# Kernel tuning notes

Measured on AMD Instinct MI355X. Metric: run time of the kernel, lower is better.

Reference implementation:

```python
import jax, jax.numpy as jnp
import numpy as np

B, C, H, W = 8, 64, 64, 64
NPTS = 4096          # points per image
FX = 32              # extra per-point features
DOUT = 256
K = 3


def setup_inputs() -> dict:
    key = jax.random.key(0)
    k1, k2, k3, k4 = jax.random.split(key, 4)
    images = jax.random.normal(k1, (B, C, H, W), dtype=jnp.float32)
    x = jax.random.normal(k2, (B * NPTS, FX), dtype=jnp.float32)
    pos = jax.random.uniform(k3, (B * NPTS, 2), dtype=jnp.float32)
    batch = jnp.repeat(jnp.arange(B, dtype=jnp.int64), NPTS)
    W_nn = jax.random.normal(k4, (C + FX, DOUT), dtype=jnp.float32) / np.sqrt(C + FX)
    b_nn = jnp.zeros((DOUT,), dtype=jnp.float32)
    return {"images": images, "x": x, "pos": pos, "batch": batch,
            "W_nn": W_nn, "b_nn": b_nn, "k": K}


def reference(images, x, pos, batch, W_nn, b_nn, k):
    Bn, Cn, Hn, Wn = images.shape
    D = Hn
    P = D * D  # pixels per image
    # pixel features: [B, P, C]
    pix = jnp.transpose(images, (0, 2, 3, 1)).reshape(Bn, P, Cn)
    # pixel centers; flattened index i = r*D + c -> (centers[c], centers[r])
    centers = (jnp.arange(D, dtype=images.dtype) + 0.5) / D
    ppos = jnp.stack([jnp.tile(centers, D), jnp.repeat(centers, D)], axis=-1)  # [P, 2]
    # points are uniform per batch: [B, Npts, 2]
    pts = pos.reshape(Bn, -1, 2)
    # squared distances via |a|^2 + |b|^2 - 2 a.b -> [B, Npts, P]
    d2 = (jnp.sum(pts * pts, -1)[:, :, None]
          + jnp.sum(ppos * ppos, -1)[None, None, :]
          - 2.0 * jnp.einsum('bnd,pd->bnp', pts, ppos))
    neg_d2k, idx = jax.lax.top_k(-d2, k)            # k nearest pixels
    d2k = jnp.maximum(-neg_d2k, 1e-16)
    w = 1.0 / d2k                                    # [B, Npts, k]
    gathered = jax.vmap(lambda p, i: p[i])(pix, idx)  # [B, Npts, k, C]
    interp = jnp.sum(w[..., None] * gathered, axis=2) / jnp.sum(w, axis=2)[..., None]
    interp = interp.reshape(Bn * pts.shape[1], Cn)   # [N, C]
    h = jnp.concatenate([interp, x], axis=1)         # [N, C+FX]
    return h @ W_nn + b_nn                           # [N, DOUT]
```

## Files before the change

kernel.cpp:

```cpp
#include <hip/hip_runtime.h>
#include <hip/hip_bf16.h>

#define DD    64
#define PP    4096
#define NPTS  4096
#define NB    8
#define CCH   64
#define FXF   32
#define KIN   96
#define DOUT  256
#define NTOT  (NB*NPTS)

#define MTILE  64
#define HSTR   100
#define WCHUNK 16

__global__ __launch_bounds__(256) void k_transpose(const float* __restrict__ img,
                                                   float* __restrict__ pix)
{
    __shared__ float tile[32][33];
    const int b  = blockIdx.z;
    const int p0 = blockIdx.x * 32;
    const int c0 = blockIdx.y * 32;
    const int tx = threadIdx.x, ty = threadIdx.y;

    const float* src = img + (size_t)b * CCH * PP;
    float*       dst = pix + (size_t)b * PP * CCH;

#pragma unroll
    for (int i = 0; i < 32; i += 8)
        tile[ty + i][tx] = src[(size_t)(c0 + ty + i) * PP + (p0 + tx)];
    __syncthreads();
#pragma unroll
    for (int i = 0; i < 32; i += 8)
        dst[(size_t)(p0 + ty + i) * CCH + (c0 + tx)] = tile[tx][ty + i];
}

__global__ __launch_bounds__(256) void k_fused(const float* __restrict__ pix,
                                               const float* __restrict__ x,
                                               const float* __restrict__ pos,
                                               const float* __restrict__ Wn,
                                               const float* __restrict__ bn,
                                               float* __restrict__ out)
{
    __shared__ float h_lds[MTILE][HSTR];
    __shared__ float w_lds[WCHUNK][DOUT];

    const int t   = threadIdx.x;
    const int pt0 = blockIdx.x * MTILE;

    {
        const int lp  = t >> 2;
        const int q   = t & 3;
        const int gpt = pt0 + lp;
        const float px = pos[2 * gpt + 0];
        const float py = pos[2 * gpt + 1];
        const int   b  = gpt >> 12;

        const float spt = __fadd_rn(__fmul_rn(px, px), __fmul_rn(py, py));

        int cc = (int)floorf(px * 64.0f); cc = min(max(cc, 0), DD - 1);
        int rr = (int)floorf(py * 64.0f); rr = min(max(rr, 0), DD - 1);
        const int c0 = min(max(cc - 1, 0), DD - 3);
        const int r0 = min(max(rr - 1, 0), DD - 3);

        float bd0 = 1e30f, bd1 = 1e30f, bd2 = 1e30f;
        int   bp0 = 0,     bp1 = 0,     bp2 = 0;
#pragma unroll
        for (int dr = 0; dr < 3; ++dr) {
            const int   r  = r0 + dr;
            const float cy = ((float)r + 0.5f) * 0.015625f;
#pragma unroll
            for (int dc = 0; dc < 3; ++dc) {
                const int   c  = c0 + dc;
                const float cx = ((float)c + 0.5f) * 0.015625f;
                const float spp = __fadd_rn(__fmul_rn(cx, cx), __fmul_rn(cy, cy));
                const float dt  = __fmaf_rn(py, cy, __fmul_rn(px, cx));
                const float d2  = __fsub_rn(__fadd_rn(spt, spp), __fmul_rn(2.0f, dt));
                const int   p   = r * DD + c;
                if (d2 < bd2) {
                    if (d2 < bd1) {
                        if (d2 < bd0) { bd2 = bd1; bp2 = bp1; bd1 = bd0; bp1 = bp0; bd0 = d2; bp0 = p; }
                        else          { bd2 = bd1; bp2 = bp1; bd1 = d2;  bp1 = p; }
                    } else            { bd2 = d2;  bp2 = p; }
                }
            }
        }

        const float w0 = 1.0f / fmaxf(bd0, 1e-16f);
        const float w1 = 1.0f / fmaxf(bd1, 1e-16f);
        const float w2 = 1.0f / fmaxf(bd2, 1e-16f);
        const float inv = 1.0f / (w0 + w1 + w2);

        const float* g0p = pix + ((size_t)(b * PP + bp0)) * CCH + q * 16;
        const float* g1p = pix + ((size_t)(b * PP + bp1)) * CCH + q * 16;
        const float* g2p = pix + ((size_t)(b * PP + bp2)) * CCH + q * 16;
#pragma unroll
        for (int m = 0; m < 4; ++m) {
            const float4 g0 = ((const float4*)g0p)[m];
            const float4 g1 = ((const float4*)g1p)[m];
            const float4 g2 = ((const float4*)g2p)[m];
            float4 s;
            s.x = (w0 * g0.x + w1 * g1.x + w2 * g2.x) * inv;
            s.y = (w0 * g0.y + w1 * g1.y + w2 * g2.y) * inv;
            s.z = (w0 * g0.z + w1 * g1.z + w2 * g2.z) * inv;
            s.w = (w0 * g0.w + w1 * g1.w + w2 * g2.w) * inv;
            *(float4*)&h_lds[lp][q * 16 + m * 4] = s;
        }
        const float* xr = x + (size_t)gpt * FXF + q * 8;
        const float4 xa = ((const float4*)xr)[0];
        const float4 xb = ((const float4*)xr)[1];
        *(float4*)&h_lds[lp][CCH + q * 8 + 0] = xa;
        *(float4*)&h_lds[lp][CCH + q * 8 + 4] = xb;
    }
    __syncthreads();

    const int tx = t & 63;
    const int ty = t >> 6;

    float4 acc[16];
#pragma unroll
    for (int i = 0; i < 16; ++i) acc[i] = make_float4(0.f, 0.f, 0.f, 0.f);

    const float4 bias = *(const float4*)(bn + tx * 4);

    for (int k0 = 0; k0 < KIN; k0 += WCHUNK) {
        __syncthreads();
        const float4* wsrc = (const float4*)(Wn + (size_t)k0 * DOUT);
#pragma unroll
        for (int j = 0; j < 4; ++j)
            ((float4*)&w_lds[0][0])[t + 256 * j] = wsrc[t + 256 * j];
        __syncthreads();

#pragma unroll
        for (int kk = 0; kk < WCHUNK; kk += 4) {
            const float4 wv0 = *(const float4*)&w_lds[kk + 0][tx * 4];
            const float4 wv1 = *(const float4*)&w_lds[kk + 1][tx * 4];
            const float4 wv2 = *(const float4*)&w_lds[kk + 2][tx * 4];
            const float4 wv3 = *(const float4*)&w_lds[kk + 3][tx * 4];
#pragma unroll
            for (int i = 0; i < 16; ++i) {
                const float4 hv = *(const float4*)&h_lds[ty * 16 + i][k0 + kk];
                acc[i].x = fmaf(hv.x, wv0.x, fmaf(hv.y, wv1.x, fmaf(hv.z, wv2.x, fmaf(hv.w, wv3.x, acc[i].x))));
                acc[i].y = fmaf(hv.x, wv0.y, fmaf(hv.y, wv1.y, fmaf(hv.z, wv2.y, fmaf(hv.w, wv3.y, acc[i].y))));
                acc[i].z = fmaf(hv.x, wv0.z, fmaf(hv.y, wv1.z, fmaf(hv.z, wv2.z, fmaf(hv.w, wv3.z, acc[i].z))));
                acc[i].w = fmaf(hv.x, wv0.w, fmaf(hv.y, wv1.w, fmaf(hv.z, wv2.w, fmaf(hv.w, wv3.w, acc[i].w))));
            }
        }
    }

#pragma unroll
    for (int i = 0; i < 16; ++i) {
        float4 o;
        o.x = acc[i].x + bias.x; o.y = acc[i].y + bias.y;
        o.z = acc[i].z + bias.z; o.w = acc[i].w + bias.w;
        *(float4*)(out + ((size_t)(pt0 + ty * 16 + i)) * DOUT + tx * 4) = o;
    }
}

extern "C" void kernel_launch(void* const* d_in, const int* in_sizes, int n_in,
                              void* d_out, int out_size, void* d_ws, size_t ws_size,
                              hipStream_t stream)
{
    const float* images = (const float*)d_in[0];
    const float* x      = (const float*)d_in[1];
    const float* pos    = (const float*)d_in[2];
    const float* W_nn   = (const float*)d_in[4];
    const float* b_nn   = (const float*)d_in[5];
    float* out = (float*)d_out;

    float* pix = (float*)d_ws;

    k_transpose<<<dim3(PP / 32, CCH / 32, NB), dim3(32, 8), 0, stream>>>(images, pix);
    k_fused<<<NTOT / MTILE, 256, 0, stream>>>(pix, x, pos, W_nn, b_nn, out);
}
```

Measured before the change: 109.3 us.

## Use 512-thread fused blocks with register-prefetched weights and wider transpose tiles

The fused kernel now runs 512 threads per 64-point tile, halving per-thread gather work and accumulator registers (8 rows instead of 16). The next weight chunk is held in registers and prefetched while the current chunk is used, and one __syncthreads is folded into the loop. The transpose kernel now moves 64x64 tiles with float4 loads, and position loads are vectorised to float2. The aim is more resident waves and hidden global latency, at the cost of more threads each doing less work and the same LDS-bound inner loop.

```diff
diff --git a/kernel.cpp b/kernel.cpp
--- a/kernel.cpp
+++ b/kernel.cpp
@@ -14,47 +14,58 @@
 #define MTILE  64
 #define HSTR   100
 #define WCHUNK 16
+#define NCHUNK (KIN / WCHUNK)
 
 __global__ __launch_bounds__(256) void k_transpose(const float* __restrict__ img,
                                                    float* __restrict__ pix)
 {
-    __shared__ float tile[32][33];
+    __shared__ float tile[64][65];
     const int b  = blockIdx.z;
-    const int p0 = blockIdx.x * 32;
-    const int c0 = blockIdx.y * 32;
-    const int tx = threadIdx.x, ty = threadIdx.y;
+    const int p0 = blockIdx.x * 64;
+    const int t  = threadIdx.x;
 
     const float* src = img + (size_t)b * CCH * PP;
     float*       dst = pix + (size_t)b * PP * CCH;
 
+    {
+        const int p4 = t & 15;
+        const int ch = t >> 4;
 #pragma unroll
-    for (int i = 0; i < 32; i += 8)
-        tile[ty + i][tx] = src[(size_t)(c0 + ty + i) * PP + (p0 + tx)];
+        for (int i = 0; i < 64; i += 16) {
+            const float4 v = ((const float4*)(src + (size_t)(ch + i) * PP + p0))[p4];
+            *(float4*)&tile[ch + i][p4 * 4] = v;
+        }
+    }
     __syncthreads();
+    {
+        const int ch = t & 63;
+        const int py = t >> 6;
 #pragma unroll
-    for (int i = 0; i < 32; i += 8)
-        dst[(size_t)(p0 + ty + i) * CCH + (c0 + tx)] = tile[tx][ty + i];
+        for (int i = 0; i < 64; i += 4)
+            dst[(size_t)(p0 + py + i) * CCH + ch] = tile[ch][py + i];
+    }
 }
 
-__global__ __launch_bounds__(256) void k_fused(const float* __restrict__ pix,
-                                               const float* __restrict__ x,
-                                               const float* __restrict__ pos,
-                                               const float* __restrict__ Wn,
-                                               const float* __restrict__ bn,
-                                               float* __restrict__ out)
+__global__ __launch_bounds__(512, 4) void k_fused(const float* __restrict__ pix,
+                                                  const float* __restrict__ x,
+                                                  const float* __restrict__ pos,
+                                                  const float* __restrict__ Wn,
+                                                  const float* __restrict__ bn,
+                                                  float* __restrict__ out)
 {
     __shared__ float h_lds[MTILE][HSTR];
-    __shared__ float w_lds[WCHUNK][DOUT];
+    __shared__ float w_lds[WCHUNK * DOUT];
 
     const int t   = threadIdx.x;
     const int pt0 = blockIdx.x * MTILE;
 
     {
-        const int lp  = t >> 2;
-        const int q   = t & 3;
+        const int lp  = t >> 3;
+        const int q   = t & 7;
         const int gpt = pt0 + lp;
-        const float px = pos[2 * gpt + 0];
-        const float py = pos[2 * gpt + 1];
+        const float2 pp = ((const float2*)pos)[gpt];
+        const float px = pp.x;
+        const float py = pp.y;
         const int   b  = gpt >> 12;
 
         const float spt = __fadd_rn(__fmul_rn(px, px), __fmul_rn(py, py));
@@ -92,11 +103,11 @@
         const float w2 = 1.0f / fmaxf(bd2, 1e-16f);
         const float inv = 1.0f / (w0 + w1 + w2);
 
-        const float* g0p = pix + ((size_t)(b * PP + bp0)) * CCH + q * 16;
-        const float* g1p = pix + ((size_t)(b * PP + bp1)) * CCH + q * 16;
-        const float* g2p = pix + ((size_t)(b * PP + bp2)) * CCH + q * 16;
+        const float* g0p = pix + ((size_t)(b * PP + bp0)) * CCH + q * 8;
+        const float* g1p = pix + ((size_t)(b * PP + bp1)) * CCH + q * 8;
+        const float* g2p = pix + ((size_t)(b * PP + bp2)) * CCH + q * 8;
 #pragma unroll
-        for (int m = 0; m < 4; ++m) {
+        for (int m = 0; m < 2; ++m) {
             const float4 g0 = ((const float4*)g0p)[m];
             const float4 g1 = ((const float4*)g1p)[m];
             const float4 g2 = ((const float4*)g2p)[m];
@@ -105,42 +116,45 @@
             s.y = (w0 * g0.y + w1 * g1.y + w2 * g2.y) * inv;
             s.z = (w0 * g0.z + w1 * g1.z + w2 * g2.z) * inv;
             s.w = (w0 * g0.w + w1 * g1.w + w2 * g2.w) * inv;
-            *(float4*)&h_lds[lp][q * 16 + m * 4] = s;
+            *(float4*)&h_lds[lp][q * 8 + m * 4] = s;
         }
-        const float* xr = x + (size_t)gpt * FXF + q * 8;
-        const float4 xa = ((const float4*)xr)[0];
-        const float4 xb = ((const float4*)xr)[1];
-        *(float4*)&h_lds[lp][CCH + q * 8 + 0] = xa;
-        *(float4*)&h_lds[lp][CCH + q * 8 + 4] = xb;
+        const float4 xv = *(const float4*)(x + (size_t)gpt * FXF + q * 4);
+        *(float4*)&h_lds[lp][CCH + q * 4] = xv;
     }
-    __syncthreads();
 
     const int tx = t & 63;
     const int ty = t >> 6;
 
-    float4 acc[16];
+    float4 acc[8];
 #pragma unroll
-    for (int i = 0; i < 16; ++i) acc[i] = make_float4(0.f, 0.f, 0.f, 0.f);
+    for (int i = 0; i < 8; ++i) acc[i] = make_float4(0.f, 0.f, 0.f, 0.f);
 
     const float4 bias = *(const float4*)(bn + tx * 4);
 
-    for (int k0 = 0; k0 < KIN; k0 += WCHUNK) {
+    float4 wpre0 = ((const float4*)Wn)[t];
+    float4 wpre1 = ((const float4*)Wn)[t + 512];
+
+    for (int c = 0; c < NCHUNK; ++c) {
         __syncthreads();
-        const float4* wsrc = (const float4*)(Wn + (size_t)k0 * DOUT);
-#pragma unroll
-        for (int j = 0; j < 4; ++j)
-            ((float4*)&w_lds[0][0])[t + 256 * j] = wsrc[t + 256 * j];
+        ((float4*)w_lds)[t]       = wpre0;
+        ((float4*)w_lds)[t + 512] = wpre1;
+        if (c + 1 < NCHUNK) {
+            const float4* wsrc = (const float4*)(Wn + (size_t)(c + 1) * WCHUNK * DOUT);
+            wpre0 = wsrc[t];
+            wpre1 = wsrc[t + 512];
+        }
         __syncthreads();
 
+        const int k0 = c * WCHUNK;
 #pragma unroll
         for (int kk = 0; kk < WCHUNK; kk += 4) {
-            const float4 wv0 = *(const float4*)&w_lds[kk + 0][tx * 4];
-            const float4 wv1 = *(const float4*)&w_lds[kk + 1][tx * 4];
-            const float4 wv2 = *(const float4*)&w_lds[kk + 2][tx * 4];
-            const float4 wv3 = *(const float4*)&w_lds[kk + 3][tx * 4];
+            const float4 wv0 = *(const float4*)&w_lds[(kk + 0) * DOUT + tx * 4];
+            const float4 wv1 = *(const float4*)&w_lds[(kk + 1) * DOUT + tx * 4];
+            const float4 wv2 = *(const float4*)&w_lds[(kk + 2) * DOUT + tx * 4];
+            const float4 wv3 = *(const float4*)&w_lds[(kk + 3) * DOUT + tx * 4];
 #pragma unroll
-            for (int i = 0; i < 16; ++i) {
-                const float4 hv = *(const float4*)&h_lds[ty * 16 + i][k0 + kk];
+            for (int i = 0; i < 8; ++i) {
+                const float4 hv = *(const float4*)&h_lds[ty * 8 + i][k0 + kk];
                 acc[i].x = fmaf(hv.x, wv0.x, fmaf(hv.y, wv1.x, fmaf(hv.z, wv2.x, fmaf(hv.w, wv3.x, acc[i].x))));
                 acc[i].y = fmaf(hv.x, wv0.y, fmaf(hv.y, wv1.y, fmaf(hv.z, wv2.y, fmaf(hv.w, wv3.y, acc[i].y))));
                 acc[i].z = fmaf(hv.x, wv0.z, fmaf(hv.y, wv1.z, fmaf(hv.z, wv2.z, fmaf(hv.w, wv3.z, acc[i].z))));
@@ -150,11 +164,11 @@
     }
 
 #pragma unroll
-    for (int i = 0; i < 16; ++i) {
+    for (int i = 0; i < 8; ++i) {
         float4 o;
         o.x = acc[i].x + bias.x; o.y = acc[i].y + bias.y;
         o.z = acc[i].z + bias.z; o.w = acc[i].w + bias.w;
-        *(float4*)(out + ((size_t)(pt0 + ty * 16 + i)) * DOUT + tx * 4) = o;
+        *(float4*)(out + ((size_t)(pt0 + ty * 8 + i)) * DOUT + tx * 4) = o;
     }
 }
 
@@ -171,6 +185,6 @@
 
     float* pix = (float*)d_ws;
 
-    k_transpose<<<dim3(PP / 32, CCH / 32, NB), dim3(32, 8), 0, stream>>>(images, pix);
-    k_fused<<<NTOT / MTILE, 256, 0, stream>>>(pix, x, pos, W_nn, b_nn, out);
+    k_transpose<<<dim3(PP / 64, 1, NB), 256, 0, stream>>>(images, pix);
+    k_fused<<<NTOT / MTILE, 512, 0, stream>>>(pix, x, pos, W_nn, b_nn, out);
 }
```

After: 105.2 us. 3.8% less time.
